# Optimization experiments

Measured on AMD Instinct MI355X. Metric: run time of the kernel, lower is better.

Reference implementation:

```python
import jax, jax.numpy as jnp
import numpy as np


def Qmat(V):
    """Chain of Householder reflections: Q = I @ H(v_0) @ ... @ H(v_{d-1}).

    Faithful to the source: columns of V are normalized, H(v) = I - 2 v v^T.
    M @ H(v) == M - 2 (M v) v^T, so each step is a matvec + rank-1 update
    (same math as the source's full GEMM, O(d^2) per step instead of O(d^3)).
    """
    d = V.shape[0]
    # torch.norm(V.T, 2, dim=1) == L2 norm of each column of V
    norms = jnp.linalg.norm(V, axis=0)  # (d,)
    Vn = V / norms[None, :]

    def step(M, v):
        Mv = M @ v                        # (d,)
        return M - 2.0 * jnp.outer(Mv, v), None

    M0 = jnp.eye(d, dtype=V.dtype)
    M, _ = jax.lax.scan(step, M0, Vn.T)   # iterate over columns v_i
    return M


def setup_inputs() -> dict:
    key = jax.random.key(0)
    k1, k2 = jax.random.split(key)
    ci, co = 1024, 2048
    U = 0.05 * jax.random.normal(k1, (ci, ci), dtype=jnp.float32)
    V = 0.05 * jax.random.normal(k2, (co, co), dtype=jnp.float32)
    return {"U": U, "V": V}


def reference(U, V):
    ci, co = U.shape[0], V.shape[0]
    Qu = Qmat(U)  # (ci, ci) orthogonal
    Qv = Qmat(V)  # (co, co) orthogonal
    if ci < co:
        weight = Qu @ Qv[:ci, :]      # (ci, co)
    else:
        weight = Qu[:, :co] @ Qv      # (ci, co)
    return weight
```

## Files before the change

kernel.cpp:

```cpp
#include <hip/hip_runtime.h>
#include <hip/hip_bf16.h>
#include <cstdint>

#define CI 1024
#define CO 2048
#define NB 256

typedef float  fx4  __attribute__((ext_vector_type(4)));
typedef short  s16x4 __attribute__((ext_vector_type(4)));
typedef short  s16x8 __attribute__((ext_vector_type(8)));
typedef unsigned short u16;

#define MFMA(a,b,c) __builtin_amdgcn_mfma_f32_16x16x32_bf16((a),(b),(c),0,0,0)

__device__ __forceinline__ u16 f2b(float x) {
    __hip_bfloat16 h = __float2bfloat16(x);
    return __builtin_bit_cast(u16, h);
}
__device__ __forceinline__ float b2f(u16 u) {
    __hip_bfloat16 h = __builtin_bit_cast(__hip_bfloat16, u);
    return __bfloat162float(h);
}


__global__ __launch_bounds__(256) void colnorm2(const float* __restrict__ M, float* __restrict__ n2, int d) {
    int c = blockIdx.x * 256 + threadIdx.x;
    int r0 = blockIdx.y * 64;
    float s = 0.0f;
    for (int r = r0; r < r0 + 64; ++r) {
        float v = M[(size_t)r * d + c];
        s = fmaf(v, v, s);
    }
    atomicAdd(&n2[c], s);
}

__global__ __launch_bounds__(256) void init_W(float* __restrict__ W) {
    int c = blockIdx.x * 256 + threadIdx.x;
    int r = blockIdx.y;
    W[(size_t)r * CO + c] = (c == r) ? 1.0f : 0.0f;
}

__global__ __launch_bounds__(256) void reduce_S(const float* __restrict__ src, float* __restrict__ dst, int split) {
    int b = blockIdx.y;
    int i = blockIdx.x * 256 + threadIdx.x;
    const float* p = src + (size_t)b * split * NB * NB + i;
    float acc = 0.0f;
    for (int s = 0; s < split; ++s) acc += p[(size_t)s * NB * NB];
    dst[(size_t)b * NB * NB + i] = acc;
}

__global__ __launch_bounds__(256) void trans_planes(const float* __restrict__ X, int d,
                                                    u16* __restrict__ Th, u16* __restrict__ Tl) {
    size_t zo = (size_t)blockIdx.z * d * d;
    const float* Xz = X + zo;
    u16* Thz = Th + zo;
    u16* Tlz = Tl + zo;
    __shared__ float tile[32][33];
    int t = threadIdx.x;
    int r = t >> 3, c4 = (t & 7) * 4;
    int bx = blockIdx.x, by = blockIdx.y;
    fx4 v = *(const fx4*)(Xz + (size_t)(by * 32 + r) * d + bx * 32 + c4);
    tile[r][c4 + 0] = v[0]; tile[r][c4 + 1] = v[1]; tile[r][c4 + 2] = v[2]; tile[r][c4 + 3] = v[3];
    __syncthreads();
    int a = bx * 32 + r;
    u16 h[4], l[4];
    #pragma unroll
    for (int j = 0; j < 4; ++j) {
        float f = tile[c4 + j][r];
        u16 hb = f2b(f);
        h[j] = hb;
        l[j] = f2b(f - b2f(hb));
    }
    size_t o = (size_t)a * d + by * 32 + c4;
    *(s16x4*)&Thz[o] = *(s16x4*)&h[0];
    *(s16x4*)&Tlz[o] = *(s16x4*)&l[0];
}

__global__ __launch_bounds__(256) void scale_S(float* __restrict__ S,
                                               const float* __restrict__ n2u, const float* __restrict__ n2v) {
    int j = blockIdx.x, b = blockIdx.y, i = threadIdx.x;
    const float* n2 = (b < 4) ? (n2u + b * NB) : (n2v + (size_t)(b - 4) * NB);
    float inv = (1.0f / sqrtf(n2[j])) * (1.0f / sqrtf(n2[i]));
    S[(size_t)b * NB * NB + (size_t)j * NB + i] *= inv;
}

__global__ __launch_bounds__(64) void diag_inv64(const float* __restrict__ Ssc, float* __restrict__ Tt) {
    int cg = blockIdx.x;
    int b = blockIdx.y;
    int d = cg >> 6, j = cg & 63;
    const float* S = Ssc + (size_t)b * NB * NB + (size_t)(d * 64) * NB + d * 64;
    float* Trow = Tt + (size_t)b * NB * NB + (size_t)(d * 64 + j) * NB + d * 64;
    int l = threadIdx.x;
    float x = (l == j) ? 2.0f : 0.0f;
    float a = 0.0f;
    int jpad = (j + 7) & ~7;
    float q0=0,q1=0,q2=0,q3=0,q4=0,q5=0,q6=0,q7=0;
#define LR(Q, R) { int _r = (R); if (_r >= 1 && _r <= j) Q = S[(size_t)_r * NB + l]; }
    LR(q0, jpad - 0) LR(q1, jpad - 1) LR(q2, jpad - 2) LR(q3, jpad - 3)
    LR(q4, jpad - 4) LR(q5, jpad - 5) LR(q6, jpad - 6) LR(q7, jpad - 7)
#define ST(Q) { \
    float yk = __shfl(x, k); \
    a = fmaf(Q, yk, a); \
    if (k <= j && l == k - 1) x = -2.0f * a; \
    int pr = k - 8; \
    if (pr >= 1) Q = S[(size_t)pr * NB + l]; \
    --k; }
    int k = jpad;
    int ng = jpad >> 3;
    for (int g = 0; g < ng; ++g) {
        ST(q0) ST(q1) ST(q2) ST(q3) ST(q4) ST(q5) ST(q6) ST(q7)
    }
#undef ST
#undef LR
    Trow[l] = x;
}

__global__ __launch_bounds__(128) void merge_gemm(const float* __restrict__ Ssc, float* __restrict__ Tt,
                                                  float* __restrict__ tmp, int mode) {
    int z = blockIdx.z;
    const float* A; const float* B; float* C;
    int lda, ldb, ldc, K; float sgn;
    if (mode == 0) {
        int b = z >> 1, p = z & 1; int c0 = p * 128, r0 = c0 + 64;
        A = Ssc + (size_t)b * NB * NB + (size_t)r0 * NB + c0; lda = NB;
        B = Tt  + (size_t)b * NB * NB + (size_t)c0 * NB + c0; ldb = NB;
        C = tmp + (size_t)z * 4096; ldc = 64; K = 64; sgn = 1.0f;
    } else if (mode == 1) {
        int b = z >> 1, p = z & 1; int c0 = p * 128, r0 = c0 + 64;
        A = Tt  + (size_t)b * NB * NB + (size_t)r0 * NB + r0; lda = NB;
        B = tmp + (size_t)z * 4096; ldb = 64;
        C = Tt  + (size_t)b * NB * NB + (size_t)r0 * NB + c0; ldc = NB; K = 64; sgn = -1.0f;
    } else if (mode == 2) {
        A = Ssc + (size_t)z * NB * NB + (size_t)128 * NB; lda = NB;
        B = Tt  + (size_t)z * NB * NB; ldb = NB;
        C = tmp + (size_t)z * 16384; ldc = 128; K = 128; sgn = 1.0f;
    } else {
        A = Tt  + (size_t)z * NB * NB + (size_t)128 * NB + 128; lda = NB;
        B = tmp + (size_t)z * 16384; ldb = 128;
        C = Tt  + (size_t)z * NB * NB + (size_t)128 * NB; ldc = NB; K = 128; sgn = -1.0f;
    }
    int m0 = blockIdx.y * 64, n0 = blockIdx.x * 64;
    __shared__ float As[16][64];
    __shared__ float Bs[16][64];
    int tid = threadIdx.x;
    int tm = (tid >> 4) * 8, tn = (tid & 15) * 4;
    int ar = tid >> 2, ac = (tid & 3) * 4;
    int bk = tid >> 4, bn = (tid & 15) * 4;
    float acc[8][4] = {};
    for (int k0 = 0; k0 < K; k0 += 16) {
        #pragma unroll
        for (int p = 0; p < 2; ++p) {
            int r = ar + p * 32;
            fx4 av = *(const fx4*)(A + (size_t)(m0 + r) * lda + k0 + ac);
            As[ac + 0][r] = av[0]; As[ac + 1][r] = av[1]; As[ac + 2][r] = av[2]; As[ac + 3][r] = av[3];
        }
        #pragma unroll
        for (int p = 0; p < 2; ++p) {
            int kk = bk + p * 8;
            *(fx4*)&Bs[kk][bn] = *(const fx4*)(B + (size_t)(k0 + kk) * ldb + n0 + bn);
        }
        __syncthreads();
        #pragma unroll
        for (int k = 0; k < 16; ++k) {
            fx4 alo = *(const fx4*)&As[k][tm];
            fx4 ahi = *(const fx4*)&As[k][tm + 4];
            fx4 bv  = *(const fx4*)&Bs[k][tn];
            float a[8] = {alo[0], alo[1], alo[2], alo[3], ahi[0], ahi[1], ahi[2], ahi[3]};
            float bb[4] = {bv[0], bv[1], bv[2], bv[3]};
            #pragma unroll
            for (int i = 0; i < 8; ++i)
                #pragma unroll
                for (int jj = 0; jj < 4; ++jj) acc[i][jj] = fmaf(a[i], bb[jj], acc[i][jj]);
        }
        __syncthreads();
    }
    #pragma unroll
    for (int i = 0; i < 8; ++i) {
        fx4 v = { sgn * acc[i][0], sgn * acc[i][1], sgn * acc[i][2], sgn * acc[i][3] };
        *(fx4*)(C + (size_t)(m0 + tm + i) * ldc + n0 + tn) = v;
    }
}

__global__ __launch_bounds__(256) void mt_scale(const float* __restrict__ Tt, float* __restrict__ Mt,
                                                const float* __restrict__ n2u, const float* __restrict__ n2v) {
    int j = blockIdx.x, b = blockIdx.y, i = threadIdx.x;
    const float* n2 = (b < 4) ? (n2u + b * NB) : (n2v + (size_t)(b - 4) * NB);
    float v = 0.0f;
    if (i <= j)
        v = Tt[(size_t)b * NB * NB + (size_t)j * NB + i] * (1.0f / sqrtf(n2[i])) * (1.0f / sqrtf(n2[j]));
    Mt[(size_t)b * NB * NB + (size_t)j * NB + i] = v;
}

__device__ __forceinline__ void mma_step(const u16 Ah[][40], const u16 Al[][40],
                                         const u16 Bh[][40], const u16 Bl[][40],
                                         int wr, int wc, int lane, fx4 acc[2][2]) {
    int kb = (lane >> 4) * 8;
    int rl = lane & 15;
    s16x8 ah[2], al[2], bh[2], bl[2];
    #pragma unroll
    for (int f = 0; f < 2; ++f) {
        int ra = wr * 32 + f * 16 + rl;
        s16x4 p = *(const s16x4*)&Ah[ra][kb];
        s16x4 q = *(const s16x4*)&Ah[ra][kb + 4];
        ah[f] = __builtin_shufflevector(p, q, 0,1,2,3,4,5,6,7);
        p = *(const s16x4*)&Al[ra][kb];
        q = *(const s16x4*)&Al[ra][kb + 4];
        al[f] = __builtin_shufflevector(p, q, 0,1,2,3,4,5,6,7);
        int rb = wc * 32 + f * 16 + rl;
        p = *(const s16x4*)&Bh[rb][kb];
        q = *(const s16x4*)&Bh[rb][kb + 4];
        bh[f] = __builtin_shufflevector(p, q, 0,1,2,3,4,5,6,7);
        p = *(const s16x4*)&Bl[rb][kb];
        q = *(const s16x4*)&Bl[rb][kb + 4];
        bl[f] = __builtin_shufflevector(p, q, 0,1,2,3,4,5,6,7);
    }
    #pragma unroll
    for (int i = 0; i < 2; ++i)
        #pragma unroll
        for (int j = 0; j < 2; ++j) {
            acc[i][j] = MFMA(ah[i], bh[j], acc[i][j]);
            acc[i][j] = MFMA(ah[i], bl[j], acc[i][j]);
            acc[i][j] = MFMA(al[i], bh[j], acc[i][j]);
        }
}

template<int NPART>
__device__ __forceinline__ void stage_f32(const float* __restrict__ A, int ldA, size_t pstride,
                                          int m0, int k0, int t, u16 Dh[][40], u16 Dl[][40]) {
    int row = t >> 2, kc = (t & 3) * 8;
    const float* p = A + (size_t)(m0 + row) * ldA + k0 + kc;
    fx4 v0 = *(const fx4*)p;
    fx4 v1 = *(const fx4*)(p + 4);
    #pragma unroll
    for (int s = 1; s < NPART; ++s) {
        const float* q = p + (size_t)s * pstride;
        v0 += *(const fx4*)q;
        v1 += *(const fx4*)(q + 4);
    }
    u16 h[8], l[8];
    #pragma unroll
    for (int j = 0; j < 8; ++j) {
        float f = (j < 4) ? v0[j] : v1[j - 4];
        u16 hb = f2b(f);
        h[j] = hb;
        l[j] = f2b(f - b2f(hb));
    }
    *(s16x4*)&Dh[row][kc]     = *(s16x4*)&h[0];
    *(s16x4*)&Dh[row][kc + 4] = *(s16x4*)&h[4];
    *(s16x4*)&Dl[row][kc]     = *(s16x4*)&l[0];
    *(s16x4*)&Dl[row][kc + 4] = *(s16x4*)&l[4];
}

__device__ __forceinline__ void stage_planes(const u16* __restrict__ Ph, const u16* __restrict__ Pl, int ld,
                                             int n0, int k0, int t, u16 Dh[][40], u16 Dl[][40]) {
    int row = t >> 2, kc = (t & 3) * 8;
    size_t o = (size_t)(n0 + row) * ld + k0 + kc;
    s16x4 h0 = *(const s16x4*)(Ph + o);
    s16x4 h1 = *(const s16x4*)(Ph + o + 4);
    s16x4 l0 = *(const s16x4*)(Pl + o);
    s16x4 l1 = *(const s16x4*)(Pl + o + 4);
    *(s16x4*)&Dh[row][kc]     = h0;
    *(s16x4*)&Dh[row][kc + 4] = h1;
    *(s16x4*)&Dl[row][kc]     = l0;
    *(s16x4*)&Dl[row][kc + 4] = l1;
}

__global__ __launch_bounds__(256) void gram_mfma(const u16* __restrict__ Xh, const u16* __restrict__ Xl,
                                                 int d, int split, int chunk, float* __restrict__ Sp) {
    int z = blockIdx.z;
    int zb = z / split, ks = z % split;
    int c0 = zb * NB, kb = ks * chunk;
    float* S = Sp + (size_t)z * NB * NB;
    __shared__ u16 Ah[64][40], Al[64][40], Bh[64][40], Bl[64][40];
    int t = threadIdx.x, lane = t & 63, w = t >> 6, wr = w >> 1, wc = w & 1;
    int i0 = blockIdx.y * 64, j0 = blockIdx.x * 64;
    fx4 acc[2][2] = {};
    for (int k0 = kb; k0 < kb + chunk; k0 += 32) {
        stage_planes(Xh, Xl, d, c0 + i0, k0, t, Ah, Al);
        stage_planes(Xh, Xl, d, c0 + j0, k0, t, Bh, Bl);
        __syncthreads();
        mma_step(Ah, Al, Bh, Bl, wr, wc, lane, acc);
        __syncthreads();
    }
    #pragma unroll
    for (int fr = 0; fr < 2; ++fr)
        #pragma unroll
        for (int fc = 0; fc < 2; ++fc) {
            int row = i0 + wr * 32 + fr * 16 + ((lane >> 4) << 2);
            int col = j0 + wc * 32 + fc * 16 + (lane & 15);
            #pragma unroll
            for (int r = 0; r < 4; ++r)
                S[(size_t)(row + r) * NB + col] = acc[fr][fc][r];
        }
}

__global__ __launch_bounds__(256) void tbt_mfma(const float* __restrict__ RAW, int d,
                                                const u16* __restrict__ Mh, const u16* __restrict__ Ml,
                                                u16* __restrict__ TBh, u16* __restrict__ TBl) {
    int z = blockIdx.z;
    int c0 = z * NB;
    const u16* Mhz = Mh + (size_t)z * NB * NB;
    const u16* Mlz = Ml + (size_t)z * NB * NB;
    u16* Th = TBh + (size_t)z * d * NB;
    u16* Tl = TBl + (size_t)z * d * NB;
    __shared__ u16 Ah[64][40], Al[64][40], Bh[64][40], Bl[64][40];
    int t = threadIdx.x, lane = t & 63, w = t >> 6, wr = w >> 1, wc = w & 1;
    int m0 = blockIdx.y * 64, n0 = blockIdx.x * 64;
    fx4 acc[2][2] = {};
    for (int k0 = 0; k0 < NB; k0 += 32) {
        stage_f32<1>(RAW + c0, d, 0, m0, k0, t, Ah, Al);
        stage_planes(Mhz, Mlz, NB, n0, k0, t, Bh, Bl);
        __syncthreads();
        mma_step(Ah, Al, Bh, Bl, wr, wc, lane, acc);
        __syncthreads();
    }
    #pragma unroll
    for (int fr = 0; fr < 2; ++fr)
        #pragma unroll
        for (int fc = 0; fc < 2; ++fc) {
            int row = m0 + wr * 32 + fr * 16 + ((lane >> 4) << 2);
            int col = n0 + wc * 32 + fc * 16 + (lane & 15);
            #pragma unroll
            for (int r = 0; r < 4; ++r) {
                float f = acc[fr][fc][r];
                u16 hb = f2b(f);
                Th[(size_t)(row + r) * NB + col] = hb;
                Tl[(size_t)(row + r) * NB + col] = f2b(f - b2f(hb));
            }
        }
}

__global__ __launch_bounds__(256) void chain_part_mfma(const float* __restrict__ W,
                                                       const u16* __restrict__ Bth, const u16* __restrict__ Btl,
                                                       int ldB, float* __restrict__ Cparts, int kchunk) {
    int z = blockIdx.z;
    float* C = Cparts + (size_t)z * CI * NB;
    int kb = z * kchunk;
    __shared__ u16 Ah[64][40], Al[64][40], Bh[64][40], Bl[64][40];
    int t = threadIdx.x, lane = t & 63, w = t >> 6, wr = w >> 1, wc = w & 1;
    int m0 = blockIdx.y * 64, n0 = blockIdx.x * 64;
    fx4 acc[2][2] = {};
    for (int k0 = kb; k0 < kb + kchunk; k0 += 32) {
        stage_f32<1>(W, CO, 0, m0, k0, t, Ah, Al);
        stage_planes(Bth, Btl, ldB, n0, k0, t, Bh, Bl);
        __syncthreads();
        mma_step(Ah, Al, Bh, Bl, wr, wc, lane, acc);
        __syncthreads();
    }
    #pragma unroll
    for (int fr = 0; fr < 2; ++fr)
        #pragma unroll
        for (int fc = 0; fc < 2; ++fc) {
            int row = m0 + wr * 32 + fr * 16 + ((lane >> 4) << 2);
            int col = n0 + wc * 32 + fc * 16 + (lane & 15);
            #pragma unroll
            for (int r = 0; r < 4; ++r)
                C[(size_t)(row + r) * NB + col] = acc[fr][fc][r];
        }
}

__global__ __launch_bounds__(256) void reduce_planes(const float* __restrict__ src, int npart,
                                                     u16* __restrict__ Ph, u16* __restrict__ Pl) {
    size_t idx = ((size_t)blockIdx.x * 256 + threadIdx.x) * 8;
    fx4 v0 = *(const fx4*)(src + idx);
    fx4 v1 = *(const fx4*)(src + idx + 4);
    for (int s = 1; s < npart; ++s) {
        const float* p = src + (size_t)s * CI * NB + idx;
        v0 += *(const fx4*)p;
        v1 += *(const fx4*)(p + 4);
    }
    u16 h[8], l[8];
    #pragma unroll
    for (int j = 0; j < 8; ++j) {
        float f = (j < 4) ? v0[j] : v1[j - 4];
        u16 hb = f2b(f);
        h[j] = hb;
        l[j] = f2b(f - b2f(hb));
    }
    *(s16x4*)&Ph[idx]     = *(s16x4*)&h[0];
    *(s16x4*)&Ph[idx + 4] = *(s16x4*)&h[4];
    *(s16x4*)&Pl[idx]     = *(s16x4*)&l[0];
    *(s16x4*)&Pl[idx + 4] = *(s16x4*)&l[4];
}

__global__ __launch_bounds__(256) void chain_sub_pl(const u16* __restrict__ Ph, const u16* __restrict__ Pl,
                                                    const u16* __restrict__ TBh, const u16* __restrict__ TBl,
                                                    float* __restrict__ W) {
    __shared__ u16 Ah[64][40], Al[64][40], Bh[64][40], Bl[64][40];
    int t = threadIdx.x, lane = t & 63, w = t >> 6, wr = w >> 1, wc = w & 1;
    int m0 = blockIdx.y * 64, n0 = blockIdx.x * 64;
    fx4 acc[2][2] = {};
    for (int k0 = 0; k0 < NB; k0 += 32) {
        stage_planes(Ph, Pl, NB, m0, k0, t, Ah, Al);
        stage_planes(TBh, TBl, NB, n0, k0, t, Bh, Bl);
        __syncthreads();
        mma_step(Ah, Al, Bh, Bl, wr, wc, lane, acc);
        __syncthreads();
    }
    #pragma unroll
    for (int fr = 0; fr < 2; ++fr)
        #pragma unroll
        for (int fc = 0; fc < 2; ++fc) {
            int row = m0 + wr * 32 + fr * 16 + ((lane >> 4) << 2);
            int col = n0 + wc * 32 + fc * 16 + (lane & 15);
            #pragma unroll
            for (int r = 0; r < 4; ++r) {
                float* p = W + (size_t)(row + r) * CO + col;
                *p -= acc[fr][fc][r];
            }
        }
}

template<int NPART>
__global__ __launch_bounds__(256) void chain_sub_mfma(const float* __restrict__ A, int ldA, size_t pstride,
                                                      const u16* __restrict__ TBh, const u16* __restrict__ TBl,
                                                      float* __restrict__ W) {
    __shared__ u16 Ah[64][40], Al[64][40], Bh[64][40], Bl[64][40];
    int t = threadIdx.x, lane = t & 63, w = t >> 6, wr = w >> 1, wc = w & 1;
    int m0 = blockIdx.y * 64, n0 = blockIdx.x * 64;
    fx4 acc[2][2] = {};
    for (int k0 = 0; k0 < NB; k0 += 32) {
        stage_f32<NPART>(A, ldA, pstride, m0, k0, t, Ah, Al);
        stage_planes(TBh, TBl, NB, n0, k0, t, Bh, Bl);
        __syncthreads();
        mma_step(Ah, Al, Bh, Bl, wr, wc, lane, acc);
        __syncthreads();
    }
    #pragma unroll
    for (int fr = 0; fr < 2; ++fr)
        #pragma unroll
        for (int fc = 0; fc < 2; ++fc) {
            int row = m0 + wr * 32 + fr * 16 + ((lane >> 4) << 2);
            int col = n0 + wc * 32 + fc * 16 + (lane & 15);
            #pragma unroll
            for (int r = 0; r < 4; ++r) {
                float* p = W + (size_t)(row + r) * CO + col;
                *p -= acc[fr][fc][r];
            }
        }
}

extern "C" void kernel_launch(void* const* d_in, const int* in_sizes, int n_in,
                              void* d_out, int out_size, void* d_ws, size_t ws_size,
                              hipStream_t stream) {
    const float* U = (const float*)d_in[0];
    const float* V = (const float*)d_in[1];
    float* W = (float*)d_out;

    char* ws = (char*)d_ws;
    float* P0p  = (float*)(ws);
    float* tmp  = (float*)(ws);
    float* S    = (float*)(ws + ((size_t)8  << 20));
    float* Tt   = (float*)(ws + ((size_t)11 << 20));
    u16*   Mh   = (u16*)  (ws + ((size_t)14336 << 10));
    u16*   Ml   = (u16*)  (ws + ((size_t)15872 << 10));
    u16*   Ph   = (u16*)  (ws + ((size_t)17408 << 10));
    u16*   Pl   = (u16*)  (ws + ((size_t)17920 << 10));
    u16*   TBh  = (u16*)  (ws + ((size_t)18 << 20));
    u16*   TBl  = (u16*)  (ws + ((size_t)28 << 20));
    u16*   Uth  = (u16*)  (ws + ((size_t)38 << 20));
    u16*   Utl  = (u16*)  (ws + ((size_t)40 << 20));
    u16*   Vth  = (u16*)  (ws + ((size_t)42 << 20));
    u16*   Vtl  = (u16*)  (ws + ((size_t)50 << 20));
    float* n2u  = (float*)(ws + ((size_t)58 << 20));
    float* n2v  = n2u + CI;
    float* SpU  = (float*)(ws + ((size_t)18 << 20));
    float* SpV  = (float*)(ws + ((size_t)22 << 20));

    float* Su = S;  float* Sv = S + (size_t)4 * NB * NB;
    float* Mt = S;
    u16* TBhU = TBh;                       u16* TBlU = TBl;
    u16* TBhV = TBh + (size_t)4 * CI * NB; u16* TBlV = TBl + (size_t)4 * CI * NB;

    hipMemsetAsync(n2u, 0, (CI + CO) * sizeof(float), stream);
    colnorm2<<<dim3(CI / 256, CI / 64), dim3(256), 0, stream>>>(U, n2u, CI);
    colnorm2<<<dim3(CO / 256, CO / 64), dim3(256), 0, stream>>>(V, n2v, CO);

    trans_planes<<<dim3(CI / 32, CI / 32, 1), dim3(256), 0, stream>>>(U, CI, Uth, Utl);
    trans_planes<<<dim3(CO / 32, CO / 32, 1), dim3(256), 0, stream>>>(V, CO, Vth, Vtl);

    gram_mfma<<<dim3(4, 4, 4 * 4), dim3(256), 0, stream>>>(Uth, Utl, CI, 4, CI / 4, SpU);
    gram_mfma<<<dim3(4, 4, 8 * 8), dim3(256), 0, stream>>>(Vth, Vtl, CO, 8, CO / 8, SpV);
    reduce_S<<<dim3(NB * NB / 256, 4), dim3(256), 0, stream>>>(SpU, Su, 4);
    reduce_S<<<dim3(NB * NB / 256, 8), dim3(256), 0, stream>>>(SpV, Sv, 8);

    scale_S<<<dim3(NB, 12), dim3(256), 0, stream>>>(S, n2u, n2v);
    hipMemsetAsync(Tt, 0, (size_t)12 * NB * NB * sizeof(float), stream);
    diag_inv64<<<dim3(NB, 12), dim3(64), 0, stream>>>(S, Tt);
    merge_gemm<<<dim3(1, 1, 24), dim3(128), 0, stream>>>(S, Tt, tmp, 0);
    merge_gemm<<<dim3(1, 1, 24), dim3(128), 0, stream>>>(S, Tt, tmp, 1);
    merge_gemm<<<dim3(2, 2, 12), dim3(128), 0, stream>>>(S, Tt, tmp, 2);
    merge_gemm<<<dim3(2, 2, 12), dim3(128), 0, stream>>>(S, Tt, tmp, 3);
    mt_scale<<<dim3(NB, 12), dim3(256), 0, stream>>>(Tt, Mt, n2u, n2v);

    trans_planes<<<dim3(NB / 32, NB / 32, 12), dim3(256), 0, stream>>>(Mt, NB, Mh, Ml);
    tbt_mfma<<<dim3(4, CI / 64, 4), dim3(256), 0, stream>>>(U, CI, Mh, Ml, TBhU, TBlU);
    tbt_mfma<<<dim3(4, CO / 64, 8), dim3(256), 0, stream>>>(V, CO, Mh + (size_t)4 * NB * NB,
                                                            Ml + (size_t)4 * NB * NB, TBhV, TBlV);

    init_W<<<dim3(CO / 256, CI), dim3(256), 0, stream>>>(W);

    chain_sub_mfma<1><<<dim3(CI / 64, CI / 64), dim3(256), 0, stream>>>(U, CI, 0, TBhU, TBlU, W);
    for (int ib = 1; ib < CI / NB; ++ib) {
        chain_part_mfma<<<dim3(4, CI / 64, 4), dim3(256), 0, stream>>>(
            W, Uth + (size_t)ib * NB * CI, Utl + (size_t)ib * NB * CI, CI, P0p, CI / 4);
        reduce_planes<<<dim3(CI * NB / 2048), dim3(256), 0, stream>>>(P0p, 4, Ph, Pl);
        chain_sub_pl<<<dim3(CI / 64, CI / 64), dim3(256), 0, stream>>>(
            Ph, Pl, TBhU + (size_t)ib * CI * NB, TBlU + (size_t)ib * CI * NB, W);
    }
    for (int ib = 0; ib < CO / NB; ++ib) {
        chain_part_mfma<<<dim3(4, CI / 64, 8), dim3(256), 0, stream>>>(
            W, Vth + (size_t)ib * NB * CO, Vtl + (size_t)ib * NB * CO, CO, P0p, CO / 8);
        reduce_planes<<<dim3(CI * NB / 2048), dim3(256), 0, stream>>>(P0p, 8, Ph, Pl);
        chain_sub_pl<<<dim3(CO / 64, CI / 64), dim3(256), 0, stream>>>(
            Ph, Pl, TBhV + (size_t)ib * CO * NB, TBlV + (size_t)ib * CO * NB, W);
    }
}
```

Before: 414.4 us.

## Restructure Householder chain into full-size compact-WY merge with large GEMMs

Replaces the per-256-column blocked chain (many small chain_part/reduce/chain_sub launches) with a recursive compact-WY construction. The T factor is built by hierarchical merging at sizes 64, 128, 256 and 512. Q_u and W are then produced through a handful of large split-bf16 MFMA GEMMs. Column normalisation is folded into the plane conversion, which removes the separate scale passes. The aim is to cut launch count and the serial dependency chain. The cost is larger workspace and bigger triangular T multiplies.

```diff
diff --git a/kernel.cpp b/kernel.cpp
--- a/kernel.cpp
+++ b/kernel.cpp
@@ -4,7 +4,6 @@
 
 #define CI 1024
 #define CO 2048
-#define NB 256
 
 typedef float  fx4  __attribute__((ext_vector_type(4)));
 typedef short  s16x4 __attribute__((ext_vector_type(4)));
@@ -34,161 +33,69 @@
     atomicAdd(&n2[c], s);
 }
 
-__global__ __launch_bounds__(256) void init_W(float* __restrict__ W) {
-    int c = blockIdx.x * 256 + threadIdx.x;
-    int r = blockIdx.y;
-    W[(size_t)r * CO + c] = (c == r) ? 1.0f : 0.0f;
-}
-
-__global__ __launch_bounds__(256) void reduce_S(const float* __restrict__ src, float* __restrict__ dst, int split) {
-    int b = blockIdx.y;
-    int i = blockIdx.x * 256 + threadIdx.x;
-    const float* p = src + (size_t)b * split * NB * NB + i;
-    float acc = 0.0f;
-    for (int s = 0; s < split; ++s) acc += p[(size_t)s * NB * NB];
-    dst[(size_t)b * NB * NB + i] = acc;
-}
-
-__global__ __launch_bounds__(256) void trans_planes(const float* __restrict__ X, int d,
-                                                    u16* __restrict__ Th, u16* __restrict__ Tl) {
-    size_t zo = (size_t)blockIdx.z * d * d;
-    const float* Xz = X + zo;
-    u16* Thz = Th + zo;
-    u16* Tlz = Tl + zo;
+__global__ __launch_bounds__(256) void trans_planes_n(const float* __restrict__ X, int d,
+                                                      const float* __restrict__ n2,
+                                                      u16* __restrict__ Th, u16* __restrict__ Tl) {
     __shared__ float tile[32][33];
     int t = threadIdx.x;
     int r = t >> 3, c4 = (t & 7) * 4;
     int bx = blockIdx.x, by = blockIdx.y;
-    fx4 v = *(const fx4*)(Xz + (size_t)(by * 32 + r) * d + bx * 32 + c4);
+    fx4 v = *(const fx4*)(X + (size_t)(by * 32 + r) * d + bx * 32 + c4);
     tile[r][c4 + 0] = v[0]; tile[r][c4 + 1] = v[1]; tile[r][c4 + 2] = v[2]; tile[r][c4 + 3] = v[3];
     __syncthreads();
     int a = bx * 32 + r;
+    float sc = 1.0f / sqrtf(n2[a]);
     u16 h[4], l[4];
     #pragma unroll
     for (int j = 0; j < 4; ++j) {
-        float f = tile[c4 + j][r];
+        float f = tile[c4 + j][r] * sc;
         u16 hb = f2b(f);
         h[j] = hb;
         l[j] = f2b(f - b2f(hb));
     }
     size_t o = (size_t)a * d + by * 32 + c4;
-    *(s16x4*)&Thz[o] = *(s16x4*)&h[0];
-    *(s16x4*)&Tlz[o] = *(s16x4*)&l[0];
-}
-
-__global__ __launch_bounds__(256) void scale_S(float* __restrict__ S,
-                                               const float* __restrict__ n2u, const float* __restrict__ n2v) {
-    int j = blockIdx.x, b = blockIdx.y, i = threadIdx.x;
-    const float* n2 = (b < 4) ? (n2u + b * NB) : (n2v + (size_t)(b - 4) * NB);
-    float inv = (1.0f / sqrtf(n2[j])) * (1.0f / sqrtf(n2[i]));
-    S[(size_t)b * NB * NB + (size_t)j * NB + i] *= inv;
-}
-
-__global__ __launch_bounds__(64) void diag_inv64(const float* __restrict__ Ssc, float* __restrict__ Tt) {
-    int cg = blockIdx.x;
-    int b = blockIdx.y;
-    int d = cg >> 6, j = cg & 63;
-    const float* S = Ssc + (size_t)b * NB * NB + (size_t)(d * 64) * NB + d * 64;
-    float* Trow = Tt + (size_t)b * NB * NB + (size_t)(d * 64 + j) * NB + d * 64;
-    int l = threadIdx.x;
-    float x = (l == j) ? 2.0f : 0.0f;
-    float a = 0.0f;
-    int jpad = (j + 7) & ~7;
-    float q0=0,q1=0,q2=0,q3=0,q4=0,q5=0,q6=0,q7=0;
-#define LR(Q, R) { int _r = (R); if (_r >= 1 && _r <= j) Q = S[(size_t)_r * NB + l]; }
-    LR(q0, jpad - 0) LR(q1, jpad - 1) LR(q2, jpad - 2) LR(q3, jpad - 3)
-    LR(q4, jpad - 4) LR(q5, jpad - 5) LR(q6, jpad - 6) LR(q7, jpad - 7)
-#define ST(Q) { \
-    float yk = __shfl(x, k); \
-    a = fmaf(Q, yk, a); \
-    if (k <= j && l == k - 1) x = -2.0f * a; \
-    int pr = k - 8; \
-    if (pr >= 1) Q = S[(size_t)pr * NB + l]; \
-    --k; }
-    int k = jpad;
-    int ng = jpad >> 3;
-    for (int g = 0; g < ng; ++g) {
-        ST(q0) ST(q1) ST(q2) ST(q3) ST(q4) ST(q5) ST(q6) ST(q7)
-    }
-#undef ST
-#undef LR
-    Trow[l] = x;
-}
-
-__global__ __launch_bounds__(128) void merge_gemm(const float* __restrict__ Ssc, float* __restrict__ Tt,
-                                                  float* __restrict__ tmp, int mode) {
-    int z = blockIdx.z;
-    const float* A; const float* B; float* C;
-    int lda, ldb, ldc, K; float sgn;
-    if (mode == 0) {
-        int b = z >> 1, p = z & 1; int c0 = p * 128, r0 = c0 + 64;
-        A = Ssc + (size_t)b * NB * NB + (size_t)r0 * NB + c0; lda = NB;
-        B = Tt  + (size_t)b * NB * NB + (size_t)c0 * NB + c0; ldb = NB;
-        C = tmp + (size_t)z * 4096; ldc = 64; K = 64; sgn = 1.0f;
-    } else if (mode == 1) {
-        int b = z >> 1, p = z & 1; int c0 = p * 128, r0 = c0 + 64;
-        A = Tt  + (size_t)b * NB * NB + (size_t)r0 * NB + r0; lda = NB;
-        B = tmp + (size_t)z * 4096; ldb = 64;
-        C = Tt  + (size_t)b * NB * NB + (size_t)r0 * NB + c0; ldc = NB; K = 64; sgn = -1.0f;
-    } else if (mode == 2) {
-        A = Ssc + (size_t)z * NB * NB + (size_t)128 * NB; lda = NB;
-        B = Tt  + (size_t)z * NB * NB; ldb = NB;
-        C = tmp + (size_t)z * 16384; ldc = 128; K = 128; sgn = 1.0f;
-    } else {
-        A = Tt  + (size_t)z * NB * NB + (size_t)128 * NB + 128; lda = NB;
-        B = tmp + (size_t)z * 16384; ldb = 128;
-        C = Tt  + (size_t)z * NB * NB + (size_t)128 * NB; ldc = NB; K = 128; sgn = -1.0f;
-    }
-    int m0 = blockIdx.y * 64, n0 = blockIdx.x * 64;
-    __shared__ float As[16][64];
-    __shared__ float Bs[16][64];
-    int tid = threadIdx.x;
-    int tm = (tid >> 4) * 8, tn = (tid & 15) * 4;
-    int ar = tid >> 2, ac = (tid & 3) * 4;
-    int bk = tid >> 4, bn = (tid & 15) * 4;
-    float acc[8][4] = {};
-    for (int k0 = 0; k0 < K; k0 += 16) {
-        #pragma unroll
-        for (int p = 0; p < 2; ++p) {
-            int r = ar + p * 32;
-            fx4 av = *(const fx4*)(A + (size_t)(m0 + r) * lda + k0 + ac);
-            As[ac + 0][r] = av[0]; As[ac + 1][r] = av[1]; As[ac + 2][r] = av[2]; As[ac + 3][r] = av[3];
-        }
-        #pragma unroll
-        for (int p = 0; p < 2; ++p) {
-            int kk = bk + p * 8;
-            *(fx4*)&Bs[kk][bn] = *(const fx4*)(B + (size_t)(k0 + kk) * ldb + n0 + bn);
-        }
-        __syncthreads();
-        #pragma unroll
-        for (int k = 0; k < 16; ++k) {
-            fx4 alo = *(const fx4*)&As[k][tm];
-            fx4 ahi = *(const fx4*)&As[k][tm + 4];
-            fx4 bv  = *(const fx4*)&Bs[k][tn];
-            float a[8] = {alo[0], alo[1], alo[2], alo[3], ahi[0], ahi[1], ahi[2], ahi[3]};
-            float bb[4] = {bv[0], bv[1], bv[2], bv[3]};
-            #pragma unroll
-            for (int i = 0; i < 8; ++i)
-                #pragma unroll
-                for (int jj = 0; jj < 4; ++jj) acc[i][jj] = fmaf(a[i], bb[jj], acc[i][jj]);
-        }
-        __syncthreads();
-    }
-    #pragma unroll
-    for (int i = 0; i < 8; ++i) {
-        fx4 v = { sgn * acc[i][0], sgn * acc[i][1], sgn * acc[i][2], sgn * acc[i][3] };
-        *(fx4*)(C + (size_t)(m0 + tm + i) * ldc + n0 + tn) = v;
-    }
-}
-
-__global__ __launch_bounds__(256) void mt_scale(const float* __restrict__ Tt, float* __restrict__ Mt,
-                                                const float* __restrict__ n2u, const float* __restrict__ n2v) {
-    int j = blockIdx.x, b = blockIdx.y, i = threadIdx.x;
-    const float* n2 = (b < 4) ? (n2u + b * NB) : (n2v + (size_t)(b - 4) * NB);
-    float v = 0.0f;
-    if (i <= j)
-        v = Tt[(size_t)b * NB * NB + (size_t)j * NB + i] * (1.0f / sqrtf(n2[i])) * (1.0f / sqrtf(n2[j]));
-    Mt[(size_t)b * NB * NB + (size_t)j * NB + i] = v;
+    *(s16x4*)&Th[o] = *(s16x4*)&h[0];
+    *(s16x4*)&Tl[o] = *(s16x4*)&l[0];
+}
+
+__global__ __launch_bounds__(256) void planes_n(const float* __restrict__ X, int d,
+                                                const float* __restrict__ n2,
+                                                u16* __restrict__ Ph, u16* __restrict__ Pl) {
+    size_t idx = ((size_t)blockIdx.x * 256 + threadIdx.x) * 8;
+    int c = (int)(idx & (size_t)(d - 1));
+    fx4 v0 = *(const fx4*)(X + idx);
+    fx4 v1 = *(const fx4*)(X + idx + 4);
+    u16 h[8], l[8];
+    #pragma unroll
+    for (int j = 0; j < 8; ++j) {
+        float f = ((j < 4) ? v0[j] : v1[j - 4]) * (1.0f / sqrtf(n2[c + j]));
+        u16 hb = f2b(f);
+        h[j] = hb;
+        l[j] = f2b(f - b2f(hb));
+    }
+    *(s16x4*)&Ph[idx]     = *(s16x4*)&h[0];
+    *(s16x4*)&Ph[idx + 4] = *(s16x4*)&h[4];
+    *(s16x4*)&Pl[idx]     = *(s16x4*)&l[0];
+    *(s16x4*)&Pl[idx + 4] = *(s16x4*)&l[4];
+}
+
+__global__ __launch_bounds__(256) void planes_conv(const float* __restrict__ X,
+                                                   u16* __restrict__ Ph, u16* __restrict__ Pl) {
+    size_t idx = ((size_t)blockIdx.x * 256 + threadIdx.x) * 8;
+    fx4 v0 = *(const fx4*)(X + idx);
+    fx4 v1 = *(const fx4*)(X + idx + 4);
+    u16 h[8], l[8];
+    #pragma unroll
+    for (int j = 0; j < 8; ++j) {
+        float f = (j < 4) ? v0[j] : v1[j - 4];
+        u16 hb = f2b(f);
+        h[j] = hb;
+        l[j] = f2b(f - b2f(hb));
+    }
+    *(s16x4*)&Ph[idx]     = *(s16x4*)&h[0];
+    *(s16x4*)&Ph[idx + 4] = *(s16x4*)&h[4];
+    *(s16x4*)&Pl[idx]     = *(s16x4*)&l[0];
+    *(s16x4*)&Pl[idx + 4] = *(s16x4*)&l[4];
 }
 
 __device__ __forceinline__ void mma_step(const u16 Ah[][40], const u16 Al[][40],
@@ -224,19 +131,12 @@
         }
 }
 
-template<int NPART>
-__device__ __forceinline__ void stage_f32(const float* __restrict__ A, int ldA, size_t pstride,
+__device__ __forceinline__ void stage_f32(const float* __restrict__ A, int ldA,
                                           int m0, int k0, int t, u16 Dh[][40], u16 Dl[][40]) {
     int row = t >> 2, kc = (t & 3) * 8;
     const float* p = A + (size_t)(m0 + row) * ldA + k0 + kc;
     fx4 v0 = *(const fx4*)p;
     fx4 v1 = *(const fx4*)(p + 4);
-    #pragma unroll
-    for (int s = 1; s < NPART; ++s) {
-        const float* q = p + (size_t)s * pstride;
-        v0 += *(const fx4*)q;
-        v1 += *(const fx4*)(q + 4);
-    }
     u16 h[8], l[8];
     #pragma unroll
     for (int j = 0; j < 8; ++j) {
@@ -255,63 +155,214 @@
                                              int n0, int k0, int t, u16 Dh[][40], u16 Dl[][40]) {
     int row = t >> 2, kc = (t & 3) * 8;
     size_t o = (size_t)(n0 + row) * ld + k0 + kc;
-    s16x4 h0 = *(const s16x4*)(Ph + o);
-    s16x4 h1 = *(const s16x4*)(Ph + o + 4);
-    s16x4 l0 = *(const s16x4*)(Pl + o);
-    s16x4 l1 = *(const s16x4*)(Pl + o + 4);
-    *(s16x4*)&Dh[row][kc]     = h0;
-    *(s16x4*)&Dh[row][kc + 4] = h1;
-    *(s16x4*)&Dl[row][kc]     = l0;
-    *(s16x4*)&Dl[row][kc + 4] = l1;
-}
-
-__global__ __launch_bounds__(256) void gram_mfma(const u16* __restrict__ Xh, const u16* __restrict__ Xl,
-                                                 int d, int split, int chunk, float* __restrict__ Sp) {
+    *(s16x4*)&Dh[row][kc]     = *(const s16x4*)(Ph + o);
+    *(s16x4*)&Dh[row][kc + 4] = *(const s16x4*)(Ph + o + 4);
+    *(s16x4*)&Dl[row][kc]     = *(const s16x4*)(Pl + o);
+    *(s16x4*)&Dl[row][kc + 4] = *(const s16x4*)(Pl + o + 4);
+}
+
+__global__ __launch_bounds__(256) void gram_diag(const u16* __restrict__ Uh, const u16* __restrict__ Ul,
+                                                 const u16* __restrict__ Vh, const u16* __restrict__ Vl,
+                                                 float* __restrict__ Sd) {
     int z = blockIdx.z;
-    int zb = z / split, ks = z % split;
-    int c0 = zb * NB, kb = ks * chunk;
-    float* S = Sp + (size_t)z * NB * NB;
-    __shared__ u16 Ah[64][40], Al[64][40], Bh[64][40], Bl[64][40];
+    const u16 *Ph, *Pl; int ld, K, off;
+    if (z < 16) { Ph = Uh; Pl = Ul; ld = CI; K = CI; off = 64 * z; }
+    else        { Ph = Vh; Pl = Vl; ld = CO; K = CO; off = 64 * (z - 16); }
+    float* C = Sd + (size_t)z * 4096;
+    __shared__ u16 Ah[64][40], Al[64][40], Bh_[64][40], Bl_[64][40];
     int t = threadIdx.x, lane = t & 63, w = t >> 6, wr = w >> 1, wc = w & 1;
-    int i0 = blockIdx.y * 64, j0 = blockIdx.x * 64;
     fx4 acc[2][2] = {};
-    for (int k0 = kb; k0 < kb + chunk; k0 += 32) {
-        stage_planes(Xh, Xl, d, c0 + i0, k0, t, Ah, Al);
-        stage_planes(Xh, Xl, d, c0 + j0, k0, t, Bh, Bl);
-        __syncthreads();
-        mma_step(Ah, Al, Bh, Bl, wr, wc, lane, acc);
+    for (int k0 = 0; k0 < K; k0 += 32) {
+        stage_planes(Ph, Pl, ld, off, k0, t, Ah, Al);
+        stage_planes(Ph, Pl, ld, off, k0, t, Bh_, Bl_);
+        __syncthreads();
+        mma_step(Ah, Al, Bh_, Bl_, wr, wc, lane, acc);
         __syncthreads();
     }
     #pragma unroll
     for (int fr = 0; fr < 2; ++fr)
         #pragma unroll
         for (int fc = 0; fc < 2; ++fc) {
-            int row = i0 + wr * 32 + fr * 16 + ((lane >> 4) << 2);
-            int col = j0 + wc * 32 + fc * 16 + (lane & 15);
+            int row = wr * 32 + fr * 16 + ((lane >> 4) << 2);
+            int col = wc * 32 + fc * 16 + (lane & 15);
             #pragma unroll
             for (int r = 0; r < 4; ++r)
-                S[(size_t)(row + r) * NB + col] = acc[fr][fc][r];
-        }
-}
-
-__global__ __launch_bounds__(256) void tbt_mfma(const float* __restrict__ RAW, int d,
-                                                const u16* __restrict__ Mh, const u16* __restrict__ Ml,
-                                                u16* __restrict__ TBh, u16* __restrict__ TBl) {
+                C[(size_t)(row + r) * 64 + col] = acc[fr][fc][r];
+        }
+}
+
+__global__ __launch_bounds__(256) void nt_gemm(const u16* __restrict__ Uh, const u16* __restrict__ Ul,
+                                               const u16* __restrict__ Vh, const u16* __restrict__ Vl,
+                                               int s, int npu, float* __restrict__ NtBuf) {
     int z = blockIdx.z;
-    int c0 = z * NB;
-    const u16* Mhz = Mh + (size_t)z * NB * NB;
-    const u16* Mlz = Ml + (size_t)z * NB * NB;
-    u16* Th = TBh + (size_t)z * d * NB;
-    u16* Tl = TBl + (size_t)z * d * NB;
-    __shared__ u16 Ah[64][40], Al[64][40], Bh[64][40], Bl[64][40];
+    const u16 *Ph, *Pl; int ld, K, p;
+    if (z < npu) { Ph = Uh; Pl = Ul; ld = CI; K = CI; p = z; }
+    else         { Ph = Vh; Pl = Vl; ld = CO; K = CO; p = z - npu; }
+    int c0 = 2 * s * p, r1 = c0 + s;
+    float* C = NtBuf + (size_t)z * s * s;
+    __shared__ u16 Ah[64][40], Al[64][40], Bh_[64][40], Bl_[64][40];
     int t = threadIdx.x, lane = t & 63, w = t >> 6, wr = w >> 1, wc = w & 1;
     int m0 = blockIdx.y * 64, n0 = blockIdx.x * 64;
     fx4 acc[2][2] = {};
-    for (int k0 = 0; k0 < NB; k0 += 32) {
-        stage_f32<1>(RAW + c0, d, 0, m0, k0, t, Ah, Al);
-        stage_planes(Mhz, Mlz, NB, n0, k0, t, Bh, Bl);
-        __syncthreads();
-        mma_step(Ah, Al, Bh, Bl, wr, wc, lane, acc);
+    for (int k0 = 0; k0 < K; k0 += 32) {
+        stage_planes(Ph, Pl, ld, r1 + m0, k0, t, Ah, Al);
+        stage_planes(Ph, Pl, ld, c0 + n0, k0, t, Bh_, Bl_);
+        __syncthreads();
+        mma_step(Ah, Al, Bh_, Bl_, wr, wc, lane, acc);
+        __syncthreads();
+    }
+    #pragma unroll
+    for (int fr = 0; fr < 2; ++fr)
+        #pragma unroll
+        for (int fc = 0; fc < 2; ++fc) {
+            int row = m0 + wr * 32 + fr * 16 + ((lane >> 4) << 2);
+            int col = n0 + wc * 32 + fc * 16 + (lane & 15);
+            #pragma unroll
+            for (int r = 0; r < 4; ++r)
+                C[(size_t)(row + r) * s + col] = acc[fr][fc][r];
+        }
+}
+
+__global__ __launch_bounds__(64) void diag_inv64(const float* __restrict__ Sd,
+                                                 float* __restrict__ Ttu, float* __restrict__ Ttv) {
+    int j = blockIdx.x;
+    int y = blockIdx.y;
+    const float* S = Sd + (size_t)y * 4096;
+    float* T; int ldT, off;
+    if (y < 16) { T = Ttu; ldT = CI; off = 64 * y; }
+    else        { T = Ttv; ldT = CO; off = 64 * (y - 16); }
+    float* Trow = T + (size_t)(off + j) * ldT + off;
+    int l = threadIdx.x;
+    float x = (l == j) ? 2.0f : 0.0f;
+    float a = 0.0f;
+    int jpad = (j + 7) & ~7;
+    float q0=0,q1=0,q2=0,q3=0,q4=0,q5=0,q6=0,q7=0;
+#define LR(Q, R) { int _r = (R); if (_r >= 1 && _r <= j) Q = S[(size_t)_r * 64 + l]; }
+    LR(q0, jpad - 0) LR(q1, jpad - 1) LR(q2, jpad - 2) LR(q3, jpad - 3)
+    LR(q4, jpad - 4) LR(q5, jpad - 5) LR(q6, jpad - 6) LR(q7, jpad - 7)
+#define ST(Q) { \
+    float yk = __shfl(x, k); \
+    a = fmaf(Q, yk, a); \
+    if (k <= j && l == k - 1) x = -2.0f * a; \
+    int pr = k - 8; \
+    if (pr >= 1) Q = S[(size_t)pr * 64 + l]; \
+    --k; }
+    int k = jpad;
+    int ng = jpad >> 3;
+    for (int g = 0; g < ng; ++g) {
+        ST(q0) ST(q1) ST(q2) ST(q3) ST(q4) ST(q5) ST(q6) ST(q7)
+    }
+#undef ST
+#undef LR
+    Trow[l] = x;
+}
+
+__device__ __forceinline__ void fgemm_body(const float* __restrict__ A, int lda,
+                                           const float* __restrict__ B, int ldb,
+                                           float* __restrict__ C, int ldc, int K, float sgn) {
+    int m0 = blockIdx.y * 64, n0 = blockIdx.x * 64;
+    __shared__ float As[16][64];
+    __shared__ float Bs[16][64];
+    int tid = threadIdx.x;
+    int tm = (tid >> 4) * 8, tn = (tid & 15) * 4;
+    int ar = tid >> 2, ac = (tid & 3) * 4;
+    int bk = tid >> 4, bn = (tid & 15) * 4;
+    float acc[8][4] = {};
+    for (int k0 = 0; k0 < K; k0 += 16) {
+        #pragma unroll
+        for (int p = 0; p < 2; ++p) {
+            int r = ar + p * 32;
+            fx4 av = *(const fx4*)(A + (size_t)(m0 + r) * lda + k0 + ac);
+            As[ac + 0][r] = av[0]; As[ac + 1][r] = av[1]; As[ac + 2][r] = av[2]; As[ac + 3][r] = av[3];
+        }
+        #pragma unroll
+        for (int p = 0; p < 2; ++p) {
+            int kk = bk + p * 8;
+            *(fx4*)&Bs[kk][bn] = *(const fx4*)(B + (size_t)(k0 + kk) * ldb + n0 + bn);
+        }
+        __syncthreads();
+        #pragma unroll
+        for (int k = 0; k < 16; ++k) {
+            fx4 alo = *(const fx4*)&As[k][tm];
+            fx4 ahi = *(const fx4*)&As[k][tm + 4];
+            fx4 bv  = *(const fx4*)&Bs[k][tn];
+            float aa[8] = {alo[0], alo[1], alo[2], alo[3], ahi[0], ahi[1], ahi[2], ahi[3]};
+            float bb[4] = {bv[0], bv[1], bv[2], bv[3]};
+            #pragma unroll
+            for (int i = 0; i < 8; ++i)
+                #pragma unroll
+                for (int jj = 0; jj < 4; ++jj) acc[i][jj] = fmaf(aa[i], bb[jj], acc[i][jj]);
+        }
+        __syncthreads();
+    }
+    #pragma unroll
+    for (int i = 0; i < 8; ++i) {
+        fx4 v = { sgn * acc[i][0], sgn * acc[i][1], sgn * acc[i][2], sgn * acc[i][3] };
+        *(fx4*)(C + (size_t)(m0 + tm + i) * ldc + n0 + tn) = v;
+    }
+}
+
+__global__ __launch_bounds__(128) void merge_a(const float* __restrict__ NtL, int s,
+                                               const float* __restrict__ Ttu, const float* __restrict__ Ttv,
+                                               int npu, float* __restrict__ tmp) {
+    int z = blockIdx.z;
+    const float* Tt; int ldT, p;
+    if (z < npu) { Tt = Ttu; ldT = CI; p = z; } else { Tt = Ttv; ldT = CO; p = z - npu; }
+    int c0 = 2 * s * p;
+    fgemm_body(NtL + (size_t)z * s * s, s, Tt + (size_t)c0 * ldT + c0, ldT,
+               tmp + (size_t)z * s * s, s, s, 1.0f);
+}
+
+__global__ __launch_bounds__(128) void merge_b(const float* __restrict__ tmp, int s,
+                                               float* __restrict__ Ttu, float* __restrict__ Ttv, int npu) {
+    int z = blockIdx.z;
+    float* Tt; int ldT, p;
+    if (z < npu) { Tt = Ttu; ldT = CI; p = z; } else { Tt = Ttv; ldT = CO; p = z - npu; }
+    int c0 = 2 * s * p, r1 = c0 + s;
+    fgemm_body(Tt + (size_t)r1 * ldT + r1, ldT, tmp + (size_t)z * s * s, s,
+               Tt + (size_t)r1 * ldT + c0, ldT, s, -1.0f);
+}
+
+__global__ __launch_bounds__(256) void gemm_pp(const u16* __restrict__ Ah_, const u16* __restrict__ Al_, int ldA,
+                                               const u16* __restrict__ Bh0, const u16* __restrict__ Bl0, int ldB,
+                                               float* __restrict__ C, int ldC, int K) {
+    __shared__ u16 Ah[64][40], Al[64][40], Bh_[64][40], Bl_[64][40];
+    int t = threadIdx.x, lane = t & 63, w = t >> 6, wr = w >> 1, wc = w & 1;
+    int m0 = blockIdx.y * 64, n0 = blockIdx.x * 64;
+    fx4 acc[2][2] = {};
+    for (int k0 = 0; k0 < K; k0 += 32) {
+        stage_planes(Ah_, Al_, ldA, m0, k0, t, Ah, Al);
+        stage_planes(Bh0, Bl0, ldB, n0, k0, t, Bh_, Bl_);
+        __syncthreads();
+        mma_step(Ah, Al, Bh_, Bl_, wr, wc, lane, acc);
+        __syncthreads();
+    }
+    #pragma unroll
+    for (int fr = 0; fr < 2; ++fr)
+        #pragma unroll
+        for (int fc = 0; fc < 2; ++fc) {
+            int row = m0 + wr * 32 + fr * 16 + ((lane >> 4) << 2);
+            int col = n0 + wc * 32 + fc * 16 + (lane & 15);
+            #pragma unroll
+            for (int r = 0; r < 4; ++r)
+                C[(size_t)(row + r) * ldC + col] = acc[fr][fc][r];
+        }
+}
+
+template<int EPI>
+__global__ __launch_bounds__(256) void gemm_fp(const float* __restrict__ A, int ldA,
+                                               const u16* __restrict__ Bh0, const u16* __restrict__ Bl0, int ldB,
+                                               float* __restrict__ C, int ldC, int K,
+                                               const float* __restrict__ aux, int ldaux) {
+    __shared__ u16 Ah[64][40], Al[64][40], Bh_[64][40], Bl_[64][40];
+    int t = threadIdx.x, lane = t & 63, w = t >> 6, wr = w >> 1, wc = w & 1;
+    int m0 = blockIdx.y * 64, n0 = blockIdx.x * 64;
+    fx4 acc[2][2] = {};
+    for (int k0 = 0; k0 < K; k0 += 32) {
+        stage_f32(A, ldA, m0, k0, t, Ah, Al);
+        stage_planes(Bh0, Bl0, ldB, n0, k0, t, Bh_, Bl_);
+        __syncthreads();
+        mma_step(Ah, Al, Bh_, Bl_, wr, wc, lane, acc);
         __syncthreads();
     }
     #pragma unroll
@@ -322,120 +373,13 @@
             int col = n0 + wc * 32 + fc * 16 + (lane & 15);
             #pragma unroll
             for (int r = 0; r < 4; ++r) {
-                float f = acc[fr][fc][r];
-                u16 hb = f2b(f);
-                Th[(size_t)(row + r) * NB + col] = hb;
-                Tl[(size_t)(row + r) * NB + col] = f2b(f - b2f(hb));
-            }
-        }
-}
-
-__global__ __launch_bounds__(256) void chain_part_mfma(const float* __restrict__ W,
-                                                       const u16* __restrict__ Bth, const u16* __restrict__ Btl,
-                                                       int ldB, float* __restrict__ Cparts, int kchunk) {
-    int z = blockIdx.z;
-    float* C = Cparts + (size_t)z * CI * NB;
-    int kb = z * kchunk;
-    __shared__ u16 Ah[64][40], Al[64][40], Bh[64][40], Bl[64][40];
-    int t = threadIdx.x, lane = t & 63, w = t >> 6, wr = w >> 1, wc = w & 1;
-    int m0 = blockIdx.y * 64, n0 = blockIdx.x * 64;
-    fx4 acc[2][2] = {};
-    for (int k0 = kb; k0 < kb + kchunk; k0 += 32) {
-        stage_f32<1>(W, CO, 0, m0, k0, t, Ah, Al);
-        stage_planes(Bth, Btl, ldB, n0, k0, t, Bh, Bl);
-        __syncthreads();
-        mma_step(Ah, Al, Bh, Bl, wr, wc, lane, acc);
-        __syncthreads();
-    }
-    #pragma unroll
-    for (int fr = 0; fr < 2; ++fr)
-        #pragma unroll
-        for (int fc = 0; fc < 2; ++fc) {
-            int row = m0 + wr * 32 + fr * 16 + ((lane >> 4) << 2);
-            int col = n0 + wc * 32 + fc * 16 + (lane & 15);
-            #pragma unroll
-            for (int r = 0; r < 4; ++r)
-                C[(size_t)(row + r) * NB + col] = acc[fr][fc][r];
-        }
-}
-
-__global__ __launch_bounds__(256) void reduce_planes(const float* __restrict__ src, int npart,
-                                                     u16* __restrict__ Ph, u16* __restrict__ Pl) {
-    size_t idx = ((size_t)blockIdx.x * 256 + threadIdx.x) * 8;
-    fx4 v0 = *(const fx4*)(src + idx);
-    fx4 v1 = *(const fx4*)(src + idx + 4);
-    for (int s = 1; s < npart; ++s) {
-        const float* p = src + (size_t)s * CI * NB + idx;
-        v0 += *(const fx4*)p;
-        v1 += *(const fx4*)(p + 4);
-    }
-    u16 h[8], l[8];
-    #pragma unroll
-    for (int j = 0; j < 8; ++j) {
-        float f = (j < 4) ? v0[j] : v1[j - 4];
-        u16 hb = f2b(f);
-        h[j] = hb;
-        l[j] = f2b(f - b2f(hb));
-    }
-    *(s16x4*)&Ph[idx]     = *(s16x4*)&h[0];
-    *(s16x4*)&Ph[idx + 4] = *(s16x4*)&h[4];
-    *(s16x4*)&Pl[idx]     = *(s16x4*)&l[0];
-    *(s16x4*)&Pl[idx + 4] = *(s16x4*)&l[4];
-}
-
-__global__ __launch_bounds__(256) void chain_sub_pl(const u16* __restrict__ Ph, const u16* __restrict__ Pl,
-                                                    const u16* __restrict__ TBh, const u16* __restrict__ TBl,
-                                                    float* __restrict__ W) {
-    __shared__ u16 Ah[64][40], Al[64][40], Bh[64][40], Bl[64][40];
-    int t = threadIdx.x, lane = t & 63, w = t >> 6, wr = w >> 1, wc = w & 1;
-    int m0 = blockIdx.y * 64, n0 = blockIdx.x * 64;
-    fx4 acc[2][2] = {};
-    for (int k0 = 0; k0 < NB; k0 += 32) {
-        stage_planes(Ph, Pl, NB, m0, k0, t, Ah, Al);
-        stage_planes(TBh, TBl, NB, n0, k0, t, Bh, Bl);
-        __syncthreads();
-        mma_step(Ah, Al, Bh, Bl, wr, wc, lane, acc);
-        __syncthreads();
-    }
-    #pragma unroll
-    for (int fr = 0; fr < 2; ++fr)
-        #pragma unroll
-        for (int fc = 0; fc < 2; ++fc) {
-            int row = m0 + wr * 32 + fr * 16 + ((lane >> 4) << 2);
-            int col = n0 + wc * 32 + fc * 16 + (lane & 15);
-            #pragma unroll
-            for (int r = 0; r < 4; ++r) {
-                float* p = W + (size_t)(row + r) * CO + col;
-                *p -= acc[fr][fc][r];
-            }
-        }
-}
-
-template<int NPART>
-__global__ __launch_bounds__(256) void chain_sub_mfma(const float* __restrict__ A, int ldA, size_t pstride,
-                                                      const u16* __restrict__ TBh, const u16* __restrict__ TBl,
-                                                      float* __restrict__ W) {
-    __shared__ u16 Ah[64][40], Al[64][40], Bh[64][40], Bl[64][40];
-    int t = threadIdx.x, lane = t & 63, w = t >> 6, wr = w >> 1, wc = w & 1;
-    int m0 = blockIdx.y * 64, n0 = blockIdx.x * 64;
-    fx4 acc[2][2] = {};
-    for (int k0 = 0; k0 < NB; k0 += 32) {
-        stage_f32<NPART>(A, ldA, pstride, m0, k0, t, Ah, Al);
-        stage_planes(TBh, TBl, NB, n0, k0, t, Bh, Bl);
-        __syncthreads();
-        mma_step(Ah, Al, Bh, Bl, wr, wc, lane, acc);
-        __syncthreads();
-    }
-    #pragma unroll
-    for (int fr = 0; fr < 2; ++fr)
-        #pragma unroll
-        for (int fc = 0; fc < 2; ++fc) {
-            int row = m0 + wr * 32 + fr * 16 + ((lane >> 4) << 2);
-            int col = n0 + wc * 32 + fc * 16 + (lane & 15);
-            #pragma unroll
-            for (int r = 0; r < 4; ++r) {
-                float* p = W + (size_t)(row + r) * CO + col;
-                *p -= acc[fr][fc][r];
+                float a = acc[fr][fc][r];
+                float* p = C + (size_t)(row + r) * ldC + col;
+                if (EPI == 0)      *p = a;
+                else if (EPI == 1) *p = ((row + r) == col ? 1.0f : 0.0f) - a;
+                else if (EPI == 2) *p = aux[(size_t)(row + r) * ldaux + col] - a;
+                else if (EPI == 3) *p -= a;
+                else               *p = ((col < CI) ? aux[(size_t)(row + r) * ldaux + col] : 0.0f) - a;
             }
         }
 }
@@ -448,71 +392,83 @@
     float* W = (float*)d_out;
 
     char* ws = (char*)d_ws;
-    float* P0p  = (float*)(ws);
-    float* tmp  = (float*)(ws);
-    float* S    = (float*)(ws + ((size_t)8  << 20));
-    float* Tt   = (float*)(ws + ((size_t)11 << 20));
-    u16*   Mh   = (u16*)  (ws + ((size_t)14336 << 10));
-    u16*   Ml   = (u16*)  (ws + ((size_t)15872 << 10));
-    u16*   Ph   = (u16*)  (ws + ((size_t)17408 << 10));
-    u16*   Pl   = (u16*)  (ws + ((size_t)17920 << 10));
-    u16*   TBh  = (u16*)  (ws + ((size_t)18 << 20));
-    u16*   TBl  = (u16*)  (ws + ((size_t)28 << 20));
-    u16*   Uth  = (u16*)  (ws + ((size_t)38 << 20));
-    u16*   Utl  = (u16*)  (ws + ((size_t)40 << 20));
-    u16*   Vth  = (u16*)  (ws + ((size_t)42 << 20));
-    u16*   Vtl  = (u16*)  (ws + ((size_t)50 << 20));
-    float* n2u  = (float*)(ws + ((size_t)58 << 20));
+    u16*   Unth = (u16*)  (ws + ((size_t)0   << 20));
+    u16*   Untl = (u16*)  (ws + ((size_t)2   << 20));
+    u16*   Unh  = (u16*)  (ws + ((size_t)4   << 20));
+    u16*   Unl  = (u16*)  (ws + ((size_t)6   << 20));
+    u16*   Vnth = (u16*)  (ws + ((size_t)8   << 20));
+    u16*   Vntl = (u16*)  (ws + ((size_t)16  << 20));
+    u16*   Vnh  = (u16*)  (ws + ((size_t)24  << 20));
+    u16*   Vnl  = (u16*)  (ws + ((size_t)32  << 20));
+    float* Ttu  = (float*)(ws + ((size_t)40  << 20));
+    float* Ttv  = (float*)(ws + ((size_t)44  << 20));
+    u16*   Mtuh = (u16*)  (ws + ((size_t)60  << 20));
+    u16*   Mtul = (u16*)  (ws + ((size_t)62  << 20));
+    u16*   Mtvh = (u16*)  (ws + ((size_t)64  << 20));
+    u16*   Mtvl = (u16*)  (ws + ((size_t)72  << 20));
+    float* Sd   = (float*)(ws + ((size_t)80  << 20));
+    float* NtA  = (float*)(ws + ((size_t)81  << 20));
+    float* tmp  = (float*)(ws + ((size_t)86  << 20));
+    float* X1   = (float*)(ws + ((size_t)88  << 20));
+    float* Qp   = (float*)(ws + ((size_t)90  << 20));
+    float* H1u  = (float*)(ws + ((size_t)94  << 20));
+    float* H2u  = (float*)(ws + ((size_t)96  << 20));
+    float* Qu   = (float*)(ws + ((size_t)98  << 20));
+    float* H1   = (float*)(ws + ((size_t)102 << 20));
+    float* H2   = (float*)(ws + ((size_t)106 << 20));
+    float* H3   = (float*)(ws + ((size_t)110 << 20));
+    float* H4   = (float*)(ws + ((size_t)114 << 20));
+    float* n2u  = (float*)(ws + ((size_t)118 << 20));
     float* n2v  = n2u + CI;
-    float* SpU  = (float*)(ws + ((size_t)18 << 20));
-    float* SpV  = (float*)(ws + ((size_t)22 << 20));
-
-    float* Su = S;  float* Sv = S + (size_t)4 * NB * NB;
-    float* Mt = S;
-    u16* TBhU = TBh;                       u16* TBlU = TBl;
-    u16* TBhV = TBh + (size_t)4 * CI * NB; u16* TBlV = TBl + (size_t)4 * CI * NB;
+
+    float* Nt64  = NtA;
+    float* Nt128 = NtA + 98304;
+    float* Nt256 = NtA + 294912;
+    float* Nt512 = NtA + 688128;
 
     hipMemsetAsync(n2u, 0, (CI + CO) * sizeof(float), stream);
     colnorm2<<<dim3(CI / 256, CI / 64), dim3(256), 0, stream>>>(U, n2u, CI);
     colnorm2<<<dim3(CO / 256, CO / 64), dim3(256), 0, stream>>>(V, n2v, CO);
 
-    trans_planes<<<dim3(CI / 32, CI / 32, 1), dim3(256), 0, stream>>>(U, CI, Uth, Utl);
-    trans_planes<<<dim3(CO / 32, CO / 32, 1), dim3(256), 0, stream>>>(V, CO, Vth, Vtl);
-
-    gram_mfma<<<dim3(4, 4, 4 * 4), dim3(256), 0, stream>>>(Uth, Utl, CI, 4, CI / 4, SpU);
-    gram_mfma<<<dim3(4, 4, 8 * 8), dim3(256), 0, stream>>>(Vth, Vtl, CO, 8, CO / 8, SpV);
-    reduce_S<<<dim3(NB * NB / 256, 4), dim3(256), 0, stream>>>(SpU, Su, 4);
-    reduce_S<<<dim3(NB * NB / 256, 8), dim3(256), 0, stream>>>(SpV, Sv, 8);
-
-    scale_S<<<dim3(NB, 12), dim3(256), 0, stream>>>(S, n2u, n2v);
-    hipMemsetAsync(Tt, 0, (size_t)12 * NB * NB * sizeof(float), stream);
-    diag_inv64<<<dim3(NB, 12), dim3(64), 0, stream>>>(S, Tt);
-    merge_gemm<<<dim3(1, 1, 24), dim3(128), 0, stream>>>(S, Tt, tmp, 0);
-    merge_gemm<<<dim3(1, 1, 24), dim3(128), 0, stream>>>(S, Tt, tmp, 1);
-    merge_gemm<<<dim3(2, 2, 12), dim3(128), 0, stream>>>(S, Tt, tmp, 2);
-    merge_gemm<<<dim3(2, 2, 12), dim3(128), 0, stream>>>(S, Tt, tmp, 3);
-    mt_scale<<<dim3(NB, 12), dim3(256), 0, stream>>>(Tt, Mt, n2u, n2v);
-
-    trans_planes<<<dim3(NB / 32, NB / 32, 12), dim3(256), 0, stream>>>(Mt, NB, Mh, Ml);
-    tbt_mfma<<<dim3(4, CI / 64, 4), dim3(256), 0, stream>>>(U, CI, Mh, Ml, TBhU, TBlU);
-    tbt_mfma<<<dim3(4, CO / 64, 8), dim3(256), 0, stream>>>(V, CO, Mh + (size_t)4 * NB * NB,
-                                                            Ml + (size_t)4 * NB * NB, TBhV, TBlV);
-
-    init_W<<<dim3(CO / 256, CI), dim3(256), 0, stream>>>(W);
-
-    chain_sub_mfma<1><<<dim3(CI / 64, CI / 64), dim3(256), 0, stream>>>(U, CI, 0, TBhU, TBlU, W);
-    for (int ib = 1; ib < CI / NB; ++ib) {
-        chain_part_mfma<<<dim3(4, CI / 64, 4), dim3(256), 0, stream>>>(
-            W, Uth + (size_t)ib * NB * CI, Utl + (size_t)ib * NB * CI, CI, P0p, CI / 4);
-        reduce_planes<<<dim3(CI * NB / 2048), dim3(256), 0, stream>>>(P0p, 4, Ph, Pl);
-        chain_sub_pl<<<dim3(CI / 64, CI / 64), dim3(256), 0, stream>>>(
-            Ph, Pl, TBhU + (size_t)ib * CI * NB, TBlU + (size_t)ib * CI * NB, W);
-    }
-    for (int ib = 0; ib < CO / NB; ++ib) {
-        chain_part_mfma<<<dim3(4, CI / 64, 8), dim3(256), 0, stream>>>(
-            W, Vth + (size_t)ib * NB * CO, Vtl + (size_t)ib * NB * CO, CO, P0p, CO / 8);
-        reduce_planes<<<dim3(CI * NB / 2048), dim3(256), 0, stream>>>(P0p, 8, Ph, Pl);
-        chain_sub_pl<<<dim3(CO / 64, CI / 64), dim3(256), 0, stream>>>(
-            Ph, Pl, TBhV + (size_t)ib * CO * NB, TBlV + (size_t)ib * CO * NB, W);
-    }
-}
+    trans_planes_n<<<dim3(CI / 32, CI / 32), dim3(256), 0, stream>>>(U, CI, n2u, Unth, Untl);
+    trans_planes_n<<<dim3(CO / 32, CO / 32), dim3(256), 0, stream>>>(V, CO, n2v, Vnth, Vntl);
+    planes_n<<<dim3(CI * CI / 2048), dim3(256), 0, stream>>>(U, CI, n2u, Unh, Unl);
+    planes_n<<<dim3(CO * CO / 2048), dim3(256), 0, stream>>>(V, CO, n2v, Vnh, Vnl);
+
+    gram_diag<<<dim3(1, 1, 48), dim3(256), 0, stream>>>(Unth, Untl, Vnth, Vntl, Sd);
+    nt_gemm<<<dim3(1, 1, 24), dim3(256), 0, stream>>>(Unth, Untl, Vnth, Vntl, 64, 8, Nt64);
+    nt_gemm<<<dim3(2, 2, 12), dim3(256), 0, stream>>>(Unth, Untl, Vnth, Vntl, 128, 4, Nt128);
+    nt_gemm<<<dim3(4, 4, 6),  dim3(256), 0, stream>>>(Unth, Untl, Vnth, Vntl, 256, 2, Nt256);
+    nt_gemm<<<dim3(8, 8, 2),  dim3(256), 0, stream>>>(Unth, Untl, Vnth, Vntl, 512, 0, Nt512);
+
+    hipMemsetAsync(Ttu, 0, (size_t)20 << 20, stream);
+    diag_inv64<<<dim3(64, 48), dim3(64), 0, stream>>>(Sd, Ttu, Ttv);
+    merge_a<<<dim3(1, 1, 24), dim3(128), 0, stream>>>(Nt64, 64, Ttu, Ttv, 8, tmp);
+    merge_b<<<dim3(1, 1, 24), dim3(128), 0, stream>>>(tmp, 64, Ttu, Ttv, 8);
+    merge_a<<<dim3(2, 2, 12), dim3(128), 0, stream>>>(Nt128, 128, Ttu, Ttv, 4, tmp);
+    merge_b<<<dim3(2, 2, 12), dim3(128), 0, stream>>>(tmp, 128, Ttu, Ttv, 4);
+    merge_a<<<dim3(4, 4, 6),  dim3(128), 0, stream>>>(Nt256, 256, Ttu, Ttv, 2, tmp);
+    merge_b<<<dim3(4, 4, 6),  dim3(128), 0, stream>>>(tmp, 256, Ttu, Ttv, 2);
+    merge_a<<<dim3(8, 8, 2),  dim3(128), 0, stream>>>(Nt512, 512, Ttu, Ttv, 0, tmp);
+    merge_b<<<dim3(8, 8, 2),  dim3(128), 0, stream>>>(tmp, 512, Ttu, Ttv, 0);
+
+    planes_conv<<<dim3(CI * CI / 2048), dim3(256), 0, stream>>>(Ttu, Mtuh, Mtul);
+    planes_conv<<<dim3(CO * CO / 2048), dim3(256), 0, stream>>>(Ttv, Mtvh, Mtvl);
+
+    gemm_pp<<<dim3(8, 16), dim3(256), 0, stream>>>(Unh, Unl, CI, Mtuh, Mtul, CI, X1, 512, 512);
+    gemm_fp<1><<<dim3(16, 16), dim3(256), 0, stream>>>(X1, 512, Unh, Unl, CI, Qp, CI, 512, nullptr, 0);
+    gemm_fp<0><<<dim3(8, 16), dim3(256), 0, stream>>>(Qp, CI, Unth + (size_t)512 * CI, Untl + (size_t)512 * CI, CI,
+                                                      H1u, 512, CI, nullptr, 0);
+    gemm_fp<0><<<dim3(8, 16), dim3(256), 0, stream>>>(H1u, 512, Mtuh + (size_t)512 * CI + 512,
+                                                      Mtul + (size_t)512 * CI + 512, CI, H2u, 512, 512, nullptr, 0);
+    gemm_fp<2><<<dim3(16, 16), dim3(256), 0, stream>>>(H2u, 512, Unh + 512, Unl + 512, CI, Qu, CI, 512, Qp, CI);
+
+    gemm_fp<0><<<dim3(16, 16), dim3(256), 0, stream>>>(Qu, CI, Vnth, Vntl, CO, H1, CI, CI, nullptr, 0);
+    gemm_fp<0><<<dim3(16, 16), dim3(256), 0, stream>>>(H1, CI, Mtvh, Mtvl, CO, H2, CI, CI, nullptr, 0);
+    gemm_fp<4><<<dim3(32, 16), dim3(256), 0, stream>>>(H2, CI, Vnh, Vnl, CO, W, CO, CI, Qu, CI);
+    gemm_fp<0><<<dim3(16, 16), dim3(256), 0, stream>>>(W, CO, Vnth + (size_t)1024 * CO, Vntl + (size_t)1024 * CO, CO,
+                                                       H3, CI, CO, nullptr, 0);
+    gemm_fp<0><<<dim3(16, 16), dim3(256), 0, stream>>>(H3, CI, Mtvh + (size_t)1024 * CO + 1024,
+                                                       Mtvl + (size_t)1024 * CO + 1024, CO, H4, CI, CI, nullptr, 0);
+    gemm_fp<3><<<dim3(32, 16), dim3(256), 0, stream>>>(H4, CI, Vnh + 1024, Vnl + 1024, CO, W, CO, CI, nullptr, 0);
+}
```

Measured after the change: 680.2 us. 1.64x slower.
